# Kernel optimization log

Hardware: AMD Instinct MI355X
Metric: run time of the kernel (lower is better)

## Reference

```python
import jax, jax.numpy as jnp
import numpy as np

DIM, HEADS, K = 128, 4, 7
HD = DIM // HEADS


def _nbr_idx(n, k):
    # NATTEN boundary-clamped neighborhood (dilation=1): window start clamped to [0, n-k]
    i = np.arange(n)
    start = np.clip(i - k // 2, 0, n - k)
    idx = start[:, None] + np.arange(k)[None, :]          # (n, k) absolute neighbor index
    rel = idx - i[:, None] + (k - 1)                      # (n, k) index into 2k-1 rpb axis
    return jnp.asarray(idx), jnp.asarray(rel)


def _ln(x, w, b, eps=1e-5):
    mu = jnp.mean(x, -1, keepdims=True)
    var = jnp.var(x, -1, keepdims=True)
    return (x - mu) * jax.lax.rsqrt(var + eps) * w + b


def setup_inputs() -> dict:
    key = jax.random.key(0)
    ks = jax.random.split(key, 16)
    B, H, W, C = 1, 128, 128, DIM
    f = jax.random.normal
    inp = {
        'x': f(ks[0], (B, H, W, C), jnp.float32),
        'y': f(ks[1], (B, H, W, C), jnp.float32),
        'qv_w': f(ks[2], (2 * C, C), jnp.float32) * 0.02,
        'qv_b': jnp.zeros((2 * C,), jnp.float32),
        'k_w': f(ks[3], (C, C), jnp.float32) * 0.02,
        'k_b': jnp.zeros((C,), jnp.float32),
        'rpb': f(ks[4], (HEADS, 2 * K - 1, 2 * K - 1), jnp.float32) * 0.02,
        'proj_w': f(ks[5], (C, C), jnp.float32) * 0.02,
        'proj_b': jnp.zeros((C,), jnp.float32),
        'n1_w': jnp.ones((C,), jnp.float32),
        'n1_b': jnp.zeros((C,), jnp.float32),
        'n2_w': jnp.ones((C,), jnp.float32),
        'n2_b': jnp.zeros((C,), jnp.float32),
        'fc1_w': f(ks[6], (4 * C, C), jnp.float32) * 0.02,
        'fc1_b': jnp.zeros((4 * C,), jnp.float32),
        'fc2_w': f(ks[7], (C, 4 * C), jnp.float32) * 0.02,
        'fc2_b': jnp.zeros((C,), jnp.float32),
    }
    return inp


def _block(x, y, qv_w, qv_b, k_w, k_b, rpb, proj_w, proj_b,
           n1_w, n1_b, n2_w, n2_b, fc1_w, fc1_b, fc2_w, fc2_b):
    B, H, W, C = x.shape
    scale = HD ** -0.5
    # ---- CrossNat2D attention on norm1(x) vs y ----
    xn = _ln(x, n1_w, n1_b)
    qv = xn @ qv_w.T + qv_b                               # (B,H,W,2C)
    q = qv[..., :C].reshape(B, H, W, HEADS, HD) * scale
    v = qv[..., C:].reshape(B, H, W, HEADS, HD)
    k = (y @ k_w.T + k_b).reshape(B, H, W, HEADS, HD)

    idx_h, rel_h = _nbr_idx(H, K)
    idx_w, rel_w = _nbr_idx(W, K)
    # gather neighborhoods: (B, H, K, W, K, HEADS, HD)
    k_nbr = k[:, idx_h][:, :, :, idx_w]
    v_nbr = v[:, idx_h][:, :, :, idx_w]

    # attention logits over KxK neighborhood
    attn = jnp.einsum('bijhd,biajchd->bijhac', q, k_nbr)  # (B,H,W,heads,K,K)
    bias = rpb[:, rel_h][..., rel_w]                      # (heads,H,K,W,K)
    attn = attn + jnp.transpose(bias, (1, 3, 0, 2, 4))    # broadcast over B
    attn = jax.nn.softmax(attn.reshape(B, H, W, HEADS, K * K), axis=-1)
    attn = attn.reshape(B, H, W, HEADS, K, K)

    out = jnp.einsum('bijhac,biajchd->bijhd', attn, v_nbr).reshape(B, H, W, C)
    out = out @ proj_w.T + proj_b

    x = x + out
    # ---- MLP ----
    h = _ln(x, n2_w, n2_b) @ fc1_w.T + fc1_b
    h = jax.nn.gelu(h, approximate=False) @ fc2_w.T + fc2_b
    return x + h


def reference(x, y, qv_w, qv_b, k_w, k_b, rpb, proj_w, proj_b,
              n1_w, n1_b, n2_w, n2_b, fc1_w, fc1_b, fc2_w, fc2_b):
    return _block(x, y, qv_w, qv_b, k_w, k_b, rpb, proj_w, proj_b,
                  n1_w, n1_b, n2_w, n2_b, fc1_w, fc1_b, fc2_w, fc2_b)
```

## Files before the change

kernel.cpp:

```cpp
#include <hip/hip_runtime.h>
#include <hip/hip_bf16.h>


#define N_PIX 16384
#define C 128
#define HEADS 4
#define HD 32
#define HW 128

typedef __hip_bfloat16 bf16;
typedef __attribute__((ext_vector_type(8))) short bf16x8;
typedef __attribute__((ext_vector_type(4))) float f32x4;

__device__ __forceinline__ short f2bs(float f) {
    unsigned int r;
    asm("v_cvt_pk_bf16_f32 %0, %1, %2" : "=v"(r) : "v"(f), "v"(f));
    return (short)(r & 0xffff);
}
__device__ __forceinline__ unsigned int pack2(float a, float b) {
    unsigned int r;
    asm("v_cvt_pk_bf16_f32 %0, %1, %2" : "=v"(r) : "v"(a), "v"(b));
    return r;
}
__device__ __forceinline__ float bs2f(short s) {
    __hip_bfloat16_raw r; r.x = (unsigned short)s;
    return __bfloat162float(__hip_bfloat16(r));
}
__device__ __forceinline__ float gelu_f(float v) {
    const float z2 = v * (2.302236206f + 0.102943322f * v * v);
    return v / (1.f + exp2f(-z2));
}

__global__ __launch_bounds__(256) void k_wconv(
    const float* __restrict__ qv_w, const float* __restrict__ k_w,
    const float* __restrict__ proj_w, const float* __restrict__ fc1_w,
    const float* __restrict__ fc2_w,
    short* __restrict__ wqv, short* __restrict__ wk, short* __restrict__ wproj,
    short* __restrict__ wfc1, short* __restrict__ wfc2) {
    const int i = blockIdx.x * 256 + threadIdx.x;
    if (i < 32768) wqv[i] = f2bs(qv_w[i]);
    if (i < 16384) { wk[i] = f2bs(k_w[i]); wproj[i] = f2bs(proj_w[i]); }
    if (i < 65536) { wfc1[i] = f2bs(fc1_w[i]); wfc2[i] = f2bs(fc2_w[i]); }
}

__global__ __launch_bounds__(256, 4) void k_qkv(
    const float* __restrict__ x, const float* __restrict__ y,
    const short* __restrict__ wqv, const float* __restrict__ qv_b,
    const short* __restrict__ wk, const float* __restrict__ k_b,
    const float* __restrict__ n1_w, const float* __restrict__ n1_b,
    bf16* __restrict__ qb, bf16* __restrict__ vb, bf16* __restrict__ kb) {
    __shared__ float xr[16][132];
    __shared__ short xn[16][136];
    __shared__ short yl[16][136];
    __shared__ float muA[16], riA[16];
    const int t = threadIdx.x;
    const int pix0 = (blockIdx.x & 7) * 2048 + (blockIdx.x >> 3) * 16;
    for (int e = t; e < 512; e += 256) {
        const int r = e >> 5, c4 = (e & 31) * 4;
        const float4 xv = *(const float4*)(x + (size_t)(pix0 + r) * C + c4);
        *(float4*)&xr[r][c4] = xv;
        const float4 yv = *(const float4*)(y + (size_t)(pix0 + r) * C + c4);
        uint2 yp; yp.x = pack2(yv.x, yv.y); yp.y = pack2(yv.z, yv.w);
        *(uint2*)&yl[r][c4] = yp;
    }
    __syncthreads();
    {
        const int r = t >> 4, c8 = (t & 15) * 8;
        const float4 a = *(const float4*)&xr[r][c8];
        const float4 b = *(const float4*)&xr[r][c8 + 4];
        float sm = a.x + a.y + a.z + a.w + b.x + b.y + b.z + b.w;
        float sq = a.x * a.x + a.y * a.y + a.z * a.z + a.w * a.w
                 + b.x * b.x + b.y * b.y + b.z * b.z + b.w * b.w;
#pragma unroll
        for (int msk = 1; msk < 16; msk <<= 1) {
            sm += __shfl_xor(sm, msk, 64); sq += __shfl_xor(sq, msk, 64);
        }
        if ((t & 15) == 0) {
            const float mu = sm * (1.f / 128.f);
            const float var = sq * (1.f / 128.f) - mu * mu;
            muA[r] = mu; riA[r] = rsqrtf(var + 1e-5f);
        }
    }
    __syncthreads();
    for (int e = t; e < 2048; e += 256) {
        const int r = e >> 7, c = e & 127;
        xn[r][c] = f2bs((xr[r][c] - muA[r]) * riA[r] * n1_w[c] + n1_b[c]);
    }
    __syncthreads();
    const int wave = t >> 6, lane = t & 63, quad = lane >> 4, l15 = lane & 15;
    const float scale = 0.1767766952966369f;
    {
        bf16x8 aA[4];
#pragma unroll
        for (int kt = 0; kt < 4; kt++)
            aA[kt] = *(const bf16x8*)&xn[l15][kt * 32 + quad * 8];
#pragma unroll
        for (int s = 0; s < 4; s++) {
            const int n = (wave * 4 + s) * 16 + l15;
            f32x4 acc = {0.f, 0.f, 0.f, 0.f};
#pragma unroll
            for (int kt = 0; kt < 4; kt++) {
                bf16x8 b = *(const bf16x8*)&wqv[n * C + kt * 32 + quad * 8];
                acc = __builtin_amdgcn_mfma_f32_16x16x32_bf16(aA[kt], b, acc, 0, 0, 0);
            }
            const float bias = qv_b[n];
#pragma unroll
            for (int r = 0; r < 4; r++) {
                const int m = quad * 4 + r;
                const float v = acc[r] + bias;
                if (n < C) qb[(size_t)(pix0 + m) * C + n] = __float2bfloat16(v * scale);
                else       vb[(size_t)(pix0 + m) * C + (n - C)] = __float2bfloat16(v);
            }
        }
    }
    {
        bf16x8 aY[4];
#pragma unroll
        for (int kt = 0; kt < 4; kt++)
            aY[kt] = *(const bf16x8*)&yl[l15][kt * 32 + quad * 8];
        const int n0 = (wave * 2) * 16 + l15, n1 = (wave * 2 + 1) * 16 + l15;
        f32x4 a0 = {0.f, 0.f, 0.f, 0.f}, a1 = {0.f, 0.f, 0.f, 0.f};
#pragma unroll
        for (int kt = 0; kt < 4; kt++) {
            bf16x8 b0 = *(const bf16x8*)&wk[n0 * C + kt * 32 + quad * 8];
            bf16x8 b1 = *(const bf16x8*)&wk[n1 * C + kt * 32 + quad * 8];
            a0 = __builtin_amdgcn_mfma_f32_16x16x32_bf16(aY[kt], b0, a0, 0, 0, 0);
            a1 = __builtin_amdgcn_mfma_f32_16x16x32_bf16(aY[kt], b1, a1, 0, 0, 0);
        }
        const float b0s = k_b[n0], b1s = k_b[n1];
#pragma unroll
        for (int r = 0; r < 4; r++) {
            const int m = quad * 4 + r;
            kb[(size_t)(pix0 + m) * C + n0] = __float2bfloat16(a0[r] + b0s);
            kb[(size_t)(pix0 + m) * C + n1] = __float2bfloat16(a1[r] + b1s);
        }
    }
}

__global__ __launch_bounds__(512, 4) void k_fam(
    const bf16* __restrict__ qb, const bf16* __restrict__ kb,
    const bf16* __restrict__ vb, const float* __restrict__ rpb,
    const float* __restrict__ x,
    const short* __restrict__ wproj, const float* __restrict__ proj_b,
    const float* __restrict__ n2_w, const float* __restrict__ n2_b,
    const short* __restrict__ wfc1, const float* __restrict__ fc1_b,
    const short* __restrict__ wfc2, const float* __restrict__ fc2_b,
    float* __restrict__ out) {
    __shared__ short KP[19008];
    __shared__ short Vl[19008];
    __shared__ float muA[32], riA[32];
    short* const Pm  = KP;
    short* const aoL = KP;
    short* const x1b = KP + 4352;
    short* const xnb = KP + 8704;
    short* const hb  = Vl;
    const int t = threadIdx.x;
    const int wave = t >> 6, lane = t & 63, quad = lane >> 4, l15 = lane & 15;
    const int h = wave & 3, mt = wave >> 2;
    const int s_ = blockIdx.x >> 3;
    const int i0 = ((blockIdx.x & 7) * 2 + (s_ >> 5)) * 8;
    const int j0 = (s_ & 31) * 4;
    const int rs = min(max(i0 - 3, 0), 114);
    const int cs = min(max(j0 - 3, 0), 118);
    const int mA = mt * 16 + l15;
    const int pA = (i0 + (mA >> 2)) * HW + j0 + (mA & 3);
    const bf16x8 aQ = *(const bf16x8*)(qb + (size_t)pA * C + h * HD + quad * 8);
    const int nR0 = h * 16 + l15, nR1 = (h + 4) * 16 + l15;
    float xres0[4], xres1[4];
#pragma unroll
    for (int r = 0; r < 4; r++) {
        const int m = mt * 16 + quad * 4 + r;
        const int p = (i0 + (m >> 2)) * HW + j0 + (m & 3);
        xres0[r] = x[(size_t)p * C + nR0];
        xres1[r] = x[(size_t)p * C + nR1];
    }
    {
        const int seg = t & 15, r0 = t >> 4;
        const int q0 = (r0 * 13) >> 7;
        const int m0 = r0 - q0 * 10;
#pragma unroll
        for (int half = 0; half < 2; half++) {
            const bf16* __restrict__ src = half ? vb : kb;
            short* const dst = half ? Vl : KP;
            int r = r0, q = q0, rm = m0;
#pragma unroll
            for (int it = 0; it < 5; it++) {
                if (r < 140) {
                    const size_t g = (size_t)((rs + q) * HW + cs + rm) * C + seg * 8;
                    *(uint4*)&dst[r * 132 + seg * 8] = *(const uint4*)(src + g);
                }
                r += 32; q += 3; rm += 2;
                if (rm >= 10) { rm -= 10; q += 1; }
            }
        }
    }
    __syncthreads();
    f32x4 S[9];
#pragma unroll
    for (int nt = 0; nt < 9; nt++) {
        const bf16x8 bK = *(const bf16x8*)&KP[(nt * 16 + l15) * 132 + h * HD + quad * 8];
        f32x4 z = {0.f, 0.f, 0.f, 0.f};
        S[nt] = __builtin_amdgcn_mfma_f32_16x16x32_bf16(aQ, bK, z, 0, 0, 0);
    }
    const float* rpbh = rpb + h * 169;
    int aiA[9], ajA[9];
    {
        int ai = rs + (l15 >= 10 ? 1 : 0);
        int aj = cs + (l15 >= 10 ? l15 - 10 : l15);
        const int cb = cs + 10;
#pragma unroll
        for (int nt = 0; nt < 9; nt++) {
            aiA[nt] = ai; ajA[nt] = aj;
            aj += 6; ai += 1;
            if (aj >= cb) { aj -= 10; ai += 1; }
        }
    }
    float smx[4];
#pragma unroll
    for (int r = 0; r < 4; r++) {
        const int m = mt * 16 + quad * 4 + r;
        const int i = i0 + (m >> 2), j = j0 + (m & 3);
        const int shi = min(max(i - 3, 0), 121);
        const int swj = min(max(j - 3, 0), 121);
        float best = -1e30f;
#pragma unroll
        for (int nt = 0; nt < 9; nt++) {
            const int ai = aiA[nt], aj = ajA[nt];
            const bool vnb = (nt < 8) | (l15 < 12);
            const bool valid = vnb & (ai >= shi) & (ai <= shi + 6) & (aj >= swj) & (aj <= swj + 6);
            const int ri = min(max(ai - i + 6, 0), 12);
            const int rj = min(max(aj - j + 6, 0), 12);
            const float v = valid ? (S[nt][r] + rpbh[ri * 13 + rj]) : -1e30f;
            S[nt][r] = v;
            best = fmaxf(best, v);
        }
        for (int msk = 1; msk < 16; msk <<= 1) best = fmaxf(best, __shfl_xor(best, msk, 64));
        float s = 0.f;
#pragma unroll
        for (int nt = 0; nt < 9; nt++) {
            const float e = __expf(S[nt][r] - best);
            S[nt][r] = e;
            s += e;
        }
        for (int msk = 1; msk < 16; msk <<= 1) s += __shfl_xor(s, msk, 64);
        smx[r] = 1.f / s;
    }
    __syncthreads();
#pragma unroll
    for (int r = 0; r < 4; r++) {
        short* prow = &Pm[(wave * 16 + quad * 4 + r) * 144];
#pragma unroll
        for (int nt = 0; nt < 9; nt++)
            prow[nt * 16 + l15] = f2bs(S[nt][r] * smx[r]);
    }
    f32x4 O0 = {0.f, 0.f, 0.f, 0.f}, O1 = {0.f, 0.f, 0.f, 0.f};
#pragma unroll
    for (int kt = 0; kt < 4; kt++) {
        const bf16x8 aP = *(const bf16x8*)&Pm[(wave * 16 + l15) * 144 + kt * 32 + quad * 8];
#pragma unroll
        for (int nt2 = 0; nt2 < 2; nt2++) {
            const int ch = h * HD + nt2 * 16 + l15;
            const int base = (kt * 32 + quad * 8) * 132 + ch;
            bf16x8 bV;
#pragma unroll
            for (int jj = 0; jj < 8; jj++) bV[jj] = Vl[base + jj * 132];
            if (nt2 == 0) O0 = __builtin_amdgcn_mfma_f32_16x16x32_bf16(aP, bV, O0, 0, 0, 0);
            else          O1 = __builtin_amdgcn_mfma_f32_16x16x32_bf16(aP, bV, O1, 0, 0, 0);
        }
    }
    {
        const bf16x8 aP = *(const bf16x8*)&Pm[(wave * 16 + l15) * 144 + 128 + quad * 8];
#pragma unroll
        for (int nt2 = 0; nt2 < 2; nt2++) {
            const int ch = h * HD + nt2 * 16 + l15;
            bf16x8 bV = {0, 0, 0, 0, 0, 0, 0, 0};
            if (quad == 0) {
                const int base = 128 * 132 + ch;
#pragma unroll
                for (int jj = 0; jj < 8; jj++) bV[jj] = Vl[base + jj * 132];
            } else if (quad == 1) {
                const int base = 136 * 132 + ch;
#pragma unroll
                for (int jj = 0; jj < 4; jj++) bV[jj] = Vl[base + jj * 132];
            }
            if (nt2 == 0) O0 = __builtin_amdgcn_mfma_f32_16x16x32_bf16(aP, bV, O0, 0, 0, 0);
            else          O1 = __builtin_amdgcn_mfma_f32_16x16x32_bf16(aP, bV, O1, 0, 0, 0);
        }
    }
    bf16x8 wp0[4], wp1[4];
#pragma unroll
    for (int kt = 0; kt < 4; kt++) {
        wp0[kt] = *(const bf16x8*)&wproj[nR0 * C + kt * 32 + quad * 8];
        wp1[kt] = *(const bf16x8*)&wproj[nR1 * C + kt * 32 + quad * 8];
    }
    __syncthreads();
#pragma unroll
    for (int r = 0; r < 4; r++) {
        const int m = mt * 16 + quad * 4 + r;
        aoL[m * 136 + h * HD + l15] = f2bs(O0[r]);
        aoL[m * 136 + h * HD + 16 + l15] = f2bs(O1[r]);
    }
    __syncthreads();
    float x1f0[4], x1f1[4];
    {
        bf16x8 aO[4];
#pragma unroll
        for (int kt = 0; kt < 4; kt++)
            aO[kt] = *(const bf16x8*)&aoL[(mt * 16 + l15) * 136 + kt * 32 + quad * 8];
        f32x4 a0 = {0.f, 0.f, 0.f, 0.f}, a1 = {0.f, 0.f, 0.f, 0.f};
#pragma unroll
        for (int kt = 0; kt < 4; kt++) {
            a0 = __builtin_amdgcn_mfma_f32_16x16x32_bf16(aO[kt], wp0[kt], a0, 0, 0, 0);
            a1 = __builtin_amdgcn_mfma_f32_16x16x32_bf16(aO[kt], wp1[kt], a1, 0, 0, 0);
        }
        const float b0s = proj_b[nR0], b1s = proj_b[nR1];
#pragma unroll
        for (int r = 0; r < 4; r++) {
            const int m = mt * 16 + quad * 4 + r;
            const float v0 = xres0[r] + a0[r] + b0s;
            const float v1 = xres1[r] + a1[r] + b1s;
            x1f0[r] = v0; x1f1[r] = v1;
            x1b[m * 136 + nR0] = f2bs(v0);
            x1b[m * 136 + nR1] = f2bs(v1);
        }
    }
    __syncthreads();
    {
        const int r = t >> 4, c8 = (t & 15) * 8;
        const short* p = &x1b[r * 136 + c8];
        float sm = 0.f, sq = 0.f;
#pragma unroll
        for (int i2 = 0; i2 < 8; i2++) {
            const float v = bs2f(p[i2]); sm += v; sq += v * v;
        }
#pragma unroll
        for (int msk = 1; msk < 16; msk <<= 1) {
            sm += __shfl_xor(sm, msk, 64); sq += __shfl_xor(sq, msk, 64);
        }
        if ((t & 15) == 0) {
            const float mu = sm * (1.f / 128.f);
            const float var = sq * (1.f / 128.f) - mu * mu;
            muA[r] = mu; riA[r] = rsqrtf(var + 1e-5f);
        }
    }
    __syncthreads();
    for (int e = t; e < 32 * 128; e += 512) {
        const int r = e >> 7, c = e & 127;
        xnb[r * 136 + c] = f2bs((bs2f(x1b[r * 136 + c]) - muA[r]) * riA[r] * n2_w[c] + n2_b[c]);
    }
    __syncthreads();
    {
        bf16x8 aX[4];
#pragma unroll
        for (int kt = 0; kt < 4; kt++)
            aX[kt] = *(const bf16x8*)&xnb[(mt * 16 + l15) * 136 + kt * 32 + quad * 8];
#pragma unroll
        for (int a = 0; a < 4; a++) {
            const int n0 = (h + 8 * a) * 16 + l15, n1 = (h + 8 * a + 4) * 16 + l15;
            f32x4 a0 = {0.f, 0.f, 0.f, 0.f}, a1 = {0.f, 0.f, 0.f, 0.f};
#pragma unroll
            for (int kt = 0; kt < 4; kt++) {
                bf16x8 b0 = *(const bf16x8*)&wfc1[n0 * C + kt * 32 + quad * 8];
                bf16x8 b1 = *(const bf16x8*)&wfc1[n1 * C + kt * 32 + quad * 8];
                a0 = __builtin_amdgcn_mfma_f32_16x16x32_bf16(aX[kt], b0, a0, 0, 0, 0);
                a1 = __builtin_amdgcn_mfma_f32_16x16x32_bf16(aX[kt], b1, a1, 0, 0, 0);
            }
            const float b0s = fc1_b[n0], b1s = fc1_b[n1];
#pragma unroll
            for (int r = 0; r < 4; r++) {
                const int m = mt * 16 + quad * 4 + r;
                hb[m * 520 + n0] = f2bs(gelu_f(a0[r] + b0s));
                hb[m * 520 + n1] = f2bs(gelu_f(a1[r] + b1s));
            }
        }
    }
    __syncthreads();
    {
        f32x4 a0 = {0.f, 0.f, 0.f, 0.f}, a1 = {0.f, 0.f, 0.f, 0.f};
#pragma unroll
        for (int kt = 0; kt < 16; kt++) {
            const bf16x8 aP = *(const bf16x8*)&hb[(mt * 16 + l15) * 520 + kt * 32 + quad * 8];
            bf16x8 b0 = *(const bf16x8*)&wfc2[nR0 * 512 + kt * 32 + quad * 8];
            bf16x8 b1 = *(const bf16x8*)&wfc2[nR1 * 512 + kt * 32 + quad * 8];
            a0 = __builtin_amdgcn_mfma_f32_16x16x32_bf16(aP, b0, a0, 0, 0, 0);
            a1 = __builtin_amdgcn_mfma_f32_16x16x32_bf16(aP, b1, a1, 0, 0, 0);
        }
        const float b0s = fc2_b[nR0], b1s = fc2_b[nR1];
#pragma unroll
        for (int r = 0; r < 4; r++) {
            const int m = mt * 16 + quad * 4 + r;
            const int p = (i0 + (m >> 2)) * HW + j0 + (m & 3);
            out[(size_t)p * C + nR0] = a0[r] + b0s + x1f0[r];
            out[(size_t)p * C + nR1] = a1[r] + b1s + x1f1[r];
        }
    }
}

extern "C" void kernel_launch(void* const* d_in, const int* in_sizes, int n_in,
                              void* d_out, int out_size, void* d_ws, size_t ws_size,
                              hipStream_t stream) {
    const float* x      = (const float*)d_in[0];
    const float* y      = (const float*)d_in[1];
    const float* qv_w   = (const float*)d_in[2];
    const float* qv_b   = (const float*)d_in[3];
    const float* k_w    = (const float*)d_in[4];
    const float* k_b    = (const float*)d_in[5];
    const float* rpb    = (const float*)d_in[6];
    const float* proj_w = (const float*)d_in[7];
    const float* proj_b = (const float*)d_in[8];
    const float* n1_w   = (const float*)d_in[9];
    const float* n1_b   = (const float*)d_in[10];
    const float* n2_w   = (const float*)d_in[11];
    const float* n2_b   = (const float*)d_in[12];
    const float* fc1_w  = (const float*)d_in[13];
    const float* fc1_b  = (const float*)d_in[14];
    const float* fc2_w  = (const float*)d_in[15];
    const float* fc2_b  = (const float*)d_in[16];
    float* out = (float*)d_out;

    bf16* qb  = (bf16*)d_ws;
    bf16* vb  = qb + (size_t)N_PIX * C;
    bf16* kb  = vb + (size_t)N_PIX * C;
    short* wqv  = (short*)(kb + (size_t)N_PIX * C);
    short* wk   = wqv + 32768;
    short* wproj= wk + 16384;
    short* wfc1 = wproj + 16384;
    short* wfc2 = wfc1 + 65536;

    k_wconv<<<256, 256, 0, stream>>>(qv_w, k_w, proj_w, fc1_w, fc2_w,
                                     wqv, wk, wproj, wfc1, wfc2);
    k_qkv<<<1024, 256, 0, stream>>>(x, y, wqv, qv_b, wk, k_b, n1_w, n1_b,
                                    qb, vb, kb);
    k_fam<<<512, 512, 0, stream>>>(qb, kb, vb, rpb, x, wproj, proj_b, n2_w, n2_b,
                                   wfc1, fc1_b, wfc2, fc2_b, out);
}
```

Baseline: 161.1 us.

## Fuse LayerNorm and QKV projection into the attention-MLP kernel with halo recompute

```diff
diff --git a/kernel.cpp b/kernel.cpp
--- a/kernel.cpp
+++ b/kernel.cpp
@@ -43,117 +43,26 @@
     if (i < 65536) { wfc1[i] = f2bs(fc1_w[i]); wfc2[i] = f2bs(fc2_w[i]); }
 }
 
-__global__ __launch_bounds__(256, 4) void k_qkv(
+__global__ __launch_bounds__(512, 4) void k_all(
     const float* __restrict__ x, const float* __restrict__ y,
     const short* __restrict__ wqv, const float* __restrict__ qv_b,
     const short* __restrict__ wk, const float* __restrict__ k_b,
     const float* __restrict__ n1_w, const float* __restrict__ n1_b,
-    bf16* __restrict__ qb, bf16* __restrict__ vb, bf16* __restrict__ kb) {
-    __shared__ float xr[16][132];
-    __shared__ short xn[16][136];
-    __shared__ short yl[16][136];
-    __shared__ float muA[16], riA[16];
-    const int t = threadIdx.x;
-    const int pix0 = (blockIdx.x & 7) * 2048 + (blockIdx.x >> 3) * 16;
-    for (int e = t; e < 512; e += 256) {
-        const int r = e >> 5, c4 = (e & 31) * 4;
-        const float4 xv = *(const float4*)(x + (size_t)(pix0 + r) * C + c4);
-        *(float4*)&xr[r][c4] = xv;
-        const float4 yv = *(const float4*)(y + (size_t)(pix0 + r) * C + c4);
-        uint2 yp; yp.x = pack2(yv.x, yv.y); yp.y = pack2(yv.z, yv.w);
-        *(uint2*)&yl[r][c4] = yp;
-    }
-    __syncthreads();
-    {
-        const int r = t >> 4, c8 = (t & 15) * 8;
-        const float4 a = *(const float4*)&xr[r][c8];
-        const float4 b = *(const float4*)&xr[r][c8 + 4];
-        float sm = a.x + a.y + a.z + a.w + b.x + b.y + b.z + b.w;
-        float sq = a.x * a.x + a.y * a.y + a.z * a.z + a.w * a.w
-                 + b.x * b.x + b.y * b.y + b.z * b.z + b.w * b.w;
-#pragma unroll
-        for (int msk = 1; msk < 16; msk <<= 1) {
-            sm += __shfl_xor(sm, msk, 64); sq += __shfl_xor(sq, msk, 64);
-        }
-        if ((t & 15) == 0) {
-            const float mu = sm * (1.f / 128.f);
-            const float var = sq * (1.f / 128.f) - mu * mu;
-            muA[r] = mu; riA[r] = rsqrtf(var + 1e-5f);
-        }
-    }
-    __syncthreads();
-    for (int e = t; e < 2048; e += 256) {
-        const int r = e >> 7, c = e & 127;
-        xn[r][c] = f2bs((xr[r][c] - muA[r]) * riA[r] * n1_w[c] + n1_b[c]);
-    }
-    __syncthreads();
-    const int wave = t >> 6, lane = t & 63, quad = lane >> 4, l15 = lane & 15;
-    const float scale = 0.1767766952966369f;
-    {
-        bf16x8 aA[4];
-#pragma unroll
-        for (int kt = 0; kt < 4; kt++)
-            aA[kt] = *(const bf16x8*)&xn[l15][kt * 32 + quad * 8];
-#pragma unroll
-        for (int s = 0; s < 4; s++) {
-            const int n = (wave * 4 + s) * 16 + l15;
-            f32x4 acc = {0.f, 0.f, 0.f, 0.f};
-#pragma unroll
-            for (int kt = 0; kt < 4; kt++) {
-                bf16x8 b = *(const bf16x8*)&wqv[n * C + kt * 32 + quad * 8];
-                acc = __builtin_amdgcn_mfma_f32_16x16x32_bf16(aA[kt], b, acc, 0, 0, 0);
-            }
-            const float bias = qv_b[n];
-#pragma unroll
-            for (int r = 0; r < 4; r++) {
-                const int m = quad * 4 + r;
-                const float v = acc[r] + bias;
-                if (n < C) qb[(size_t)(pix0 + m) * C + n] = __float2bfloat16(v * scale);
-                else       vb[(size_t)(pix0 + m) * C + (n - C)] = __float2bfloat16(v);
-            }
-        }
-    }
-    {
-        bf16x8 aY[4];
-#pragma unroll
-        for (int kt = 0; kt < 4; kt++)
-            aY[kt] = *(const bf16x8*)&yl[l15][kt * 32 + quad * 8];
-        const int n0 = (wave * 2) * 16 + l15, n1 = (wave * 2 + 1) * 16 + l15;
-        f32x4 a0 = {0.f, 0.f, 0.f, 0.f}, a1 = {0.f, 0.f, 0.f, 0.f};
-#pragma unroll
-        for (int kt = 0; kt < 4; kt++) {
-            bf16x8 b0 = *(const bf16x8*)&wk[n0 * C + kt * 32 + quad * 8];
-            bf16x8 b1 = *(const bf16x8*)&wk[n1 * C + kt * 32 + quad * 8];
-            a0 = __builtin_amdgcn_mfma_f32_16x16x32_bf16(aY[kt], b0, a0, 0, 0, 0);
-            a1 = __builtin_amdgcn_mfma_f32_16x16x32_bf16(aY[kt], b1, a1, 0, 0, 0);
-        }
-        const float b0s = k_b[n0], b1s = k_b[n1];
-#pragma unroll
-        for (int r = 0; r < 4; r++) {
-            const int m = quad * 4 + r;
-            kb[(size_t)(pix0 + m) * C + n0] = __float2bfloat16(a0[r] + b0s);
-            kb[(size_t)(pix0 + m) * C + n1] = __float2bfloat16(a1[r] + b1s);
-        }
-    }
-}
-
-__global__ __launch_bounds__(512, 4) void k_fam(
-    const bf16* __restrict__ qb, const bf16* __restrict__ kb,
-    const bf16* __restrict__ vb, const float* __restrict__ rpb,
-    const float* __restrict__ x,
+    const float* __restrict__ rpb,
     const short* __restrict__ wproj, const float* __restrict__ proj_b,
     const float* __restrict__ n2_w, const float* __restrict__ n2_b,
     const short* __restrict__ wfc1, const float* __restrict__ fc1_b,
     const short* __restrict__ wfc2, const float* __restrict__ fc2_b,
     float* __restrict__ out) {
-    __shared__ short KP[19008];
-    __shared__ short Vl[19008];
+    __shared__ short XB[144 * 132];
+    __shared__ short YB[144 * 132];
+    __shared__ short qbuf[32 * 36];
     __shared__ float muA[32], riA[32];
-    short* const Pm  = KP;
-    short* const aoL = KP;
-    short* const x1b = KP + 4352;
-    short* const xnb = KP + 8704;
-    short* const hb  = Vl;
+    short* const Pm  = YB;
+    short* const aoL = YB;
+    short* const x1b = YB + 4352;
+    short* const xnb = YB + 8704;
+    short* const hb  = XB;
     const int t = threadIdx.x;
     const int wave = t >> 6, lane = t & 63, quad = lane >> 4, l15 = lane & 15;
     const int h = wave & 3, mt = wave >> 2;
@@ -162,10 +71,8 @@
     const int j0 = (s_ & 31) * 4;
     const int rs = min(max(i0 - 3, 0), 114);
     const int cs = min(max(j0 - 3, 0), 118);
-    const int mA = mt * 16 + l15;
-    const int pA = (i0 + (mA >> 2)) * HW + j0 + (mA & 3);
-    const bf16x8 aQ = *(const bf16x8*)(qb + (size_t)pA * C + h * HD + quad * 8);
     const int nR0 = h * 16 + l15, nR1 = (h + 4) * 16 + l15;
+    const float scale = 0.1767766952966369f;
     float xres0[4], xres1[4];
 #pragma unroll
     for (int r = 0; r < 4; r++) {
@@ -176,29 +83,121 @@
     }
     {
         const int seg = t & 15, r0 = t >> 4;
-        const int q0 = (r0 * 13) >> 7;
-        const int m0 = r0 - q0 * 10;
-#pragma unroll
-        for (int half = 0; half < 2; half++) {
-            const bf16* __restrict__ src = half ? vb : kb;
-            short* const dst = half ? Vl : KP;
-            int r = r0, q = q0, rm = m0;
-#pragma unroll
-            for (int it = 0; it < 5; it++) {
-                if (r < 140) {
-                    const size_t g = (size_t)((rs + q) * HW + cs + rm) * C + seg * 8;
-                    *(uint4*)&dst[r * 132 + seg * 8] = *(const uint4*)(src + g);
+        const int ch8 = seg * 8;
+        float w1[8], b1[8];
+        *(float4*)&w1[0] = *(const float4*)(n1_w + ch8);
+        *(float4*)&w1[4] = *(const float4*)(n1_w + ch8 + 4);
+        *(float4*)&b1[0] = *(const float4*)(n1_b + ch8);
+        *(float4*)&b1[4] = *(const float4*)(n1_b + ch8 + 4);
+        int qd = (r0 * 13) >> 7;
+        int rm = r0 - qd * 10;
+#pragma unroll
+        for (int p = 0; p < 5; p++) {
+            const int hr = r0 + p * 32;
+            if (hr < 140) {
+                const size_t gp = (size_t)((rs + qd) * HW + cs + rm) * C + ch8;
+                float xv[8], yv[8];
+                *(float4*)&xv[0] = *(const float4*)(x + gp);
+                *(float4*)&xv[4] = *(const float4*)(x + gp + 4);
+                *(float4*)&yv[0] = *(const float4*)(y + gp);
+                *(float4*)&yv[4] = *(const float4*)(y + gp + 4);
+                float sm = 0.f, sq = 0.f;
+#pragma unroll
+                for (int i2 = 0; i2 < 8; i2++) { sm += xv[i2]; sq += xv[i2] * xv[i2]; }
+#pragma unroll
+                for (int msk = 1; msk < 16; msk <<= 1) {
+                    sm += __shfl_xor(sm, msk, 64); sq += __shfl_xor(sq, msk, 64);
                 }
-                r += 32; q += 3; rm += 2;
-                if (rm >= 10) { rm -= 10; q += 1; }
-            }
-        }
-    }
-    __syncthreads();
+                const float mu = sm * (1.f / 128.f);
+                const float ri = rsqrtf(sq * (1.f / 128.f) - mu * mu + 1e-5f);
+                uint4 xp, yp;
+                xp.x = pack2((xv[0] - mu) * ri * w1[0] + b1[0], (xv[1] - mu) * ri * w1[1] + b1[1]);
+                xp.y = pack2((xv[2] - mu) * ri * w1[2] + b1[2], (xv[3] - mu) * ri * w1[3] + b1[3]);
+                xp.z = pack2((xv[4] - mu) * ri * w1[4] + b1[4], (xv[5] - mu) * ri * w1[5] + b1[5]);
+                xp.w = pack2((xv[6] - mu) * ri * w1[6] + b1[6], (xv[7] - mu) * ri * w1[7] + b1[7]);
+                yp.x = pack2(yv[0], yv[1]); yp.y = pack2(yv[2], yv[3]);
+                yp.z = pack2(yv[4], yv[5]); yp.w = pack2(yv[6], yv[7]);
+                *(uint4*)&XB[hr * 132 + ch8] = xp;
+                *(uint4*)&YB[hr * 132 + ch8] = yp;
+            }
+            qd += 3; rm += 2;
+            if (rm >= 10) { rm -= 10; qd += 1; }
+        }
+    }
+    __syncthreads();
+    {
+        const int mQ = wave >> 2;
+        const int mq = mQ * 16 + l15;
+        const int hrq = (i0 + (mq >> 2) - rs) * 10 + (j0 + (mq & 3) - cs);
+        bf16x8 aA[4];
+#pragma unroll
+        for (int kt = 0; kt < 4; kt++)
+            aA[kt] = *(const bf16x8*)&XB[hrq * 132 + kt * 32 + quad * 8];
+#pragma unroll
+        for (int s2 = 0; s2 < 2; s2++) {
+            const int n = ((wave & 3) * 2 + s2) * 16 + l15;
+            f32x4 acc = {0.f, 0.f, 0.f, 0.f};
+#pragma unroll
+            for (int kt = 0; kt < 4; kt++) {
+                bf16x8 b = *(const bf16x8*)&wqv[n * C + kt * 32 + quad * 8];
+                acc = __builtin_amdgcn_mfma_f32_16x16x32_bf16(aA[kt], b, acc, 0, 0, 0);
+            }
+            const float bias = qv_b[n];
+#pragma unroll
+            for (int r = 0; r < 4; r++)
+                qbuf[((wave >> 2) * 16 + quad * 4 + r) * 36 + n] = f2bs((acc[r] + bias) * scale);
+        }
+    }
+#pragma unroll 1
+    for (int rep = 0; rep < ((wave == 7) ? 2 : 1); rep++) {
+        const int mK = rep ? 8 : wave;
+        bf16x8 aA[4];
+#pragma unroll
+        for (int kt = 0; kt < 4; kt++)
+            aA[kt] = *(const bf16x8*)&YB[(mK * 16 + l15) * 132 + kt * 32 + quad * 8];
+#pragma unroll
+        for (int nk = 0; nk < 8; nk++) {
+            const int n = nk * 16 + l15;
+            f32x4 acc = {0.f, 0.f, 0.f, 0.f};
+#pragma unroll
+            for (int kt = 0; kt < 4; kt++) {
+                bf16x8 b = *(const bf16x8*)&wk[n * C + kt * 32 + quad * 8];
+                acc = __builtin_amdgcn_mfma_f32_16x16x32_bf16(aA[kt], b, acc, 0, 0, 0);
+            }
+            const float bias = k_b[n];
+#pragma unroll
+            for (int r = 0; r < 4; r++)
+                YB[(mK * 16 + quad * 4 + r) * 132 + n] = f2bs(acc[r] + bias);
+        }
+    }
+    __syncthreads();
+    const bf16x8 aQ = *(const bf16x8*)&qbuf[(mt * 16 + l15) * 36 + h * HD + quad * 8];
+#pragma unroll 1
+    for (int rep = 0; rep < ((wave == 6) ? 2 : 1); rep++) {
+        const int mV = rep ? 8 : wave;
+        bf16x8 aA[4];
+#pragma unroll
+        for (int kt = 0; kt < 4; kt++)
+            aA[kt] = *(const bf16x8*)&XB[(mV * 16 + l15) * 132 + kt * 32 + quad * 8];
+#pragma unroll
+        for (int nv = 0; nv < 8; nv++) {
+            const int n = nv * 16 + l15;
+            f32x4 acc = {0.f, 0.f, 0.f, 0.f};
+#pragma unroll
+            for (int kt = 0; kt < 4; kt++) {
+                bf16x8 b = *(const bf16x8*)&wqv[(C + n) * C + kt * 32 + quad * 8];
+                acc = __builtin_amdgcn_mfma_f32_16x16x32_bf16(aA[kt], b, acc, 0, 0, 0);
+            }
+            const float bias = qv_b[C + n];
+#pragma unroll
+            for (int r = 0; r < 4; r++)
+                XB[(mV * 16 + quad * 4 + r) * 132 + n] = f2bs(acc[r] + bias);
+        }
+    }
     f32x4 S[9];
 #pragma unroll
     for (int nt = 0; nt < 9; nt++) {
-        const bf16x8 bK = *(const bf16x8*)&KP[(nt * 16 + l15) * 132 + h * HD + quad * 8];
+        const bf16x8 bK = *(const bf16x8*)&YB[(nt * 16 + l15) * 132 + h * HD + quad * 8];
         f32x4 z = {0.f, 0.f, 0.f, 0.f};
         S[nt] = __builtin_amdgcn_mfma_f32_16x16x32_bf16(aQ, bK, z, 0, 0, 0);
     }
@@ -263,7 +262,7 @@
             const int base = (kt * 32 + quad * 8) * 132 + ch;
             bf16x8 bV;
 #pragma unroll
-            for (int jj = 0; jj < 8; jj++) bV[jj] = Vl[base + jj * 132];
+            for (int jj = 0; jj < 8; jj++) bV[jj] = XB[base + jj * 132];
             if (nt2 == 0) O0 = __builtin_amdgcn_mfma_f32_16x16x32_bf16(aP, bV, O0, 0, 0, 0);
             else          O1 = __builtin_amdgcn_mfma_f32_16x16x32_bf16(aP, bV, O1, 0, 0, 0);
         }
@@ -277,11 +276,11 @@
             if (quad == 0) {
                 const int base = 128 * 132 + ch;
 #pragma unroll
-                for (int jj = 0; jj < 8; jj++) bV[jj] = Vl[base + jj * 132];
+                for (int jj = 0; jj < 8; jj++) bV[jj] = XB[base + jj * 132];
             } else if (quad == 1) {
                 const int base = 136 * 132 + ch;
 #pragma unroll
-                for (int jj = 0; jj < 4; jj++) bV[jj] = Vl[base + jj * 132];
+                for (int jj = 0; jj < 4; jj++) bV[jj] = XB[base + jj * 132];
             }
             if (nt2 == 0) O0 = __builtin_amdgcn_mfma_f32_16x16x32_bf16(aP, bV, O0, 0, 0, 0);
             else          O1 = __builtin_amdgcn_mfma_f32_16x16x32_bf16(aP, bV, O1, 0, 0, 0);
@@ -418,10 +417,7 @@
     const float* fc2_b  = (const float*)d_in[16];
     float* out = (float*)d_out;
 
-    bf16* qb  = (bf16*)d_ws;
-    bf16* vb  = qb + (size_t)N_PIX * C;
-    bf16* kb  = vb + (size_t)N_PIX * C;
-    short* wqv  = (short*)(kb + (size_t)N_PIX * C);
+    short* wqv  = (short*)d_ws;
     short* wk   = wqv + 32768;
     short* wproj= wk + 16384;
     short* wfc1 = wproj + 16384;
@@ -429,8 +425,7 @@
 
     k_wconv<<<256, 256, 0, stream>>>(qv_w, k_w, proj_w, fc1_w, fc2_w,
                                      wqv, wk, wproj, wfc1, wfc2);
-    k_qkv<<<1024, 256, 0, stream>>>(x, y, wqv, qv_b, wk, k_b, n1_w, n1_b,
-                                    qb, vb, kb);
-    k_fam<<<512, 512, 0, stream>>>(qb, kb, vb, rpb, x, wproj, proj_b, n2_w, n2_b,
+    k_all<<<512, 512, 0, stream>>>(x, y, wqv, qv_b, wk, k_b, n1_w, n1_b, rpb,
+                                   wproj, proj_b, n2_w, n2_b,
                                    wfc1, fc1_b, wfc2, fc2_b, out);
 }
```

Result: slower. 183.1 us (+13.7%).
